# Performance work log

Hardware: AMD Instinct MI355X
Metric: run time of the kernel (lower is better)

Reference implementation:

```python
import jax, jax.numpy as jnp
import numpy as np

TOP_K = 2  # MoE top-k routing


def setup_inputs() -> dict:
    key = jax.random.key(0)
    ks = jax.random.split(key, 5)
    B, D, H, O, N = 8192, 3072, 128, 10, 8
    scale_g = 1.0 / np.sqrt(D)
    return {
        "x": jax.random.normal(ks[0], (B, D), dtype=jnp.float32),
        "Wg": jax.random.normal(ks[1], (D, N), dtype=jnp.float32) * scale_g,
        "bg": jnp.zeros((N,), dtype=jnp.float32),
        "W1": jax.random.normal(ks[2], (N, D, H), dtype=jnp.float32) * scale_g,
        "b1": jnp.zeros((N, H), dtype=jnp.float32),
        "W2": jax.random.normal(ks[3], (N, H, O), dtype=jnp.float32) * (1.0 / np.sqrt(H)),
        "b2": jnp.zeros((N, O), dtype=jnp.float32),
    }


def reference(x, Wg, bg, W1, b1, W2, b2):
    # Gating: logits -> top-k -> softmax over the k selected logits
    g = x @ Wg + bg                                  # [B, N]
    tv, ti = jax.lax.top_k(g, TOP_K)                 # [B, k]
    w = jax.nn.softmax(tv, axis=-1)                  # [B, k]
    # Expert MLPs, computed densely over all experts (vectorized dispatch)
    h = jax.nn.relu(jnp.einsum('bd,edh->beh', x, W1) + b1)   # [B, N, H]
    y = jnp.einsum('beh,eho->beo', h, W2) + b2               # [B, N, O]
    # Combine: gather each token's k selected expert outputs, weight, sum
    ysel = jnp.take_along_axis(y, ti[:, :, None], axis=1)    # [B, k, O]
    return jnp.sum(w[:, :, None] * ysel, axis=1)             # [B, O]
```

## Files before the change

### kernel.cpp

```cpp
#include <hip/hip_runtime.h>
#include <hip/hip_bf16.h>

#define B_TOK 8192
#define D_DIM 3072
#define H_DIM 128
#define O_DIM 10
#define N_EXP 8

#define BM 128
#define BK2 128
#define HLDS_STRIDE 136
#define ESTRIDE 4096

typedef __bf16 bf16x8 __attribute__((ext_vector_type(8)));
typedef float  f32x4  __attribute__((ext_vector_type(4)));
typedef unsigned short us8 __attribute__((ext_vector_type(8)));

__device__ __forceinline__ unsigned short f2bf(float f) {
  unsigned int u = __float_as_uint(f);
  unsigned int r = (u + 0x7FFFu + ((u >> 16) & 1u)) >> 16;
  return (unsigned short)r;
}

__device__ __forceinline__ void async16(const void* g, void* l) {
  __builtin_amdgcn_global_load_lds(
      (const __attribute__((address_space(1))) void*)g,
      (__attribute__((address_space(3))) void*)l,
      16, 0, 0);
}

__global__ __launch_bounds__(256) void k0_w1_transpose(const float* __restrict__ W1,
                                                       unsigned short* __restrict__ w1t) {
  __shared__ __align__(16) unsigned short lds[64 * 72];
  const int e  = blockIdx.z;
  const int d0 = blockIdx.x * 64;
  const int h0 = blockIdx.y * 64;
  const int tid = threadIdx.x;

  const float* src = W1 + ((size_t)e * D_DIM + d0) * H_DIM + h0;
  const int hl = tid & 63;
  const int dg = tid >> 6;
#pragma unroll
  for (int k = 0; k < 16; ++k) {
    const int d = dg + 4 * k;
    lds[hl * 72 + d] = f2bf(src[(size_t)d * H_DIM + hl]);
  }
  __syncthreads();

  unsigned short* dst = w1t + ((size_t)e * H_DIM + h0) * D_DIM + d0;
  const int q  = tid & 7;
  const int h1 = tid >> 3;
#pragma unroll
  for (int k = 0; k < 2; ++k) {
    const int h = h1 + 32 * k;
    const int d = q * 8;
    us8 v = *(const us8*)(lds + h * 72 + d);
    *(us8*)(dst + (size_t)h * D_DIM + d) = v;
  }
}

__global__ __launch_bounds__(256) void k1_gate(
    const float* __restrict__ x, const float* __restrict__ Wg,
    const float* __restrict__ bg,
    unsigned short* __restrict__ xb,
    int4* __restrict__ idx4, float2* __restrict__ wts,
    int* __restrict__ cnt, int* __restrict__ tlist) {
  __shared__ int lcnt[N_EXP], gbase[N_EXP];
  const int tid  = threadIdx.x;
  if (tid < N_EXP) lcnt[tid] = 0;
  __syncthreads();

  const int lane = tid & 63;
  const int wv   = tid >> 6;
  const int t0   = blockIdx.x * 16 + wv * 4;

  const float* xr0 = x + (size_t)(t0 + 0) * D_DIM;
  const float* xr1 = x + (size_t)(t0 + 1) * D_DIM;
  const float* xr2 = x + (size_t)(t0 + 2) * D_DIM;
  const float* xr3 = x + (size_t)(t0 + 3) * D_DIM;
  unsigned short* xw0 = xb + (size_t)(t0 + 0) * D_DIM;
  unsigned short* xw1 = xb + (size_t)(t0 + 1) * D_DIM;
  unsigned short* xw2 = xb + (size_t)(t0 + 2) * D_DIM;
  unsigned short* xw3 = xb + (size_t)(t0 + 3) * D_DIM;

  float acc[4][N_EXP];
#pragma unroll
  for (int t = 0; t < 4; ++t)
#pragma unroll
    for (int n = 0; n < N_EXP; ++n) acc[t][n] = 0.f;

  for (int grp = 0; grp < 3; ++grp) {
    float4 xv0[4], xv1[4], xv2[4], xv3[4];
#pragma unroll
    for (int s = 0; s < 4; ++s) {
      const int dl = (grp * 4 + s) * 256 + lane * 4;
      xv0[s] = *(const float4*)(xr0 + dl);
      xv1[s] = *(const float4*)(xr1 + dl);
      xv2[s] = *(const float4*)(xr2 + dl);
      xv3[s] = *(const float4*)(xr3 + dl);
    }
#pragma unroll
    for (int s = 0; s < 4; ++s) {
      const int dl = (grp * 4 + s) * 256 + lane * 4;
      const float4* wp = (const float4*)(Wg + (size_t)dl * N_EXP);
      float4 wa[4], wb[4];
#pragma unroll
      for (int j = 0; j < 4; ++j) { wa[j] = wp[2 * j]; wb[j] = wp[2 * j + 1]; }

      ushort4 p;
      p.x = f2bf(xv0[s].x); p.y = f2bf(xv0[s].y); p.z = f2bf(xv0[s].z); p.w = f2bf(xv0[s].w);
      *(ushort4*)(xw0 + dl) = p;
      p.x = f2bf(xv1[s].x); p.y = f2bf(xv1[s].y); p.z = f2bf(xv1[s].z); p.w = f2bf(xv1[s].w);
      *(ushort4*)(xw1 + dl) = p;
      p.x = f2bf(xv2[s].x); p.y = f2bf(xv2[s].y); p.z = f2bf(xv2[s].z); p.w = f2bf(xv2[s].w);
      *(ushort4*)(xw2 + dl) = p;
      p.x = f2bf(xv3[s].x); p.y = f2bf(xv3[s].y); p.z = f2bf(xv3[s].z); p.w = f2bf(xv3[s].w);
      *(ushort4*)(xw3 + dl) = p;

      float xe0[4] = {xv0[s].x, xv0[s].y, xv0[s].z, xv0[s].w};
      float xe1[4] = {xv1[s].x, xv1[s].y, xv1[s].z, xv1[s].w};
      float xe2[4] = {xv2[s].x, xv2[s].y, xv2[s].z, xv2[s].w};
      float xe3[4] = {xv3[s].x, xv3[s].y, xv3[s].z, xv3[s].w};
#pragma unroll
      for (int j = 0; j < 4; ++j) {
        acc[0][0] = fmaf(xe0[j], wa[j].x, acc[0][0]);
        acc[0][1] = fmaf(xe0[j], wa[j].y, acc[0][1]);
        acc[0][2] = fmaf(xe0[j], wa[j].z, acc[0][2]);
        acc[0][3] = fmaf(xe0[j], wa[j].w, acc[0][3]);
        acc[0][4] = fmaf(xe0[j], wb[j].x, acc[0][4]);
        acc[0][5] = fmaf(xe0[j], wb[j].y, acc[0][5]);
        acc[0][6] = fmaf(xe0[j], wb[j].z, acc[0][6]);
        acc[0][7] = fmaf(xe0[j], wb[j].w, acc[0][7]);
        acc[1][0] = fmaf(xe1[j], wa[j].x, acc[1][0]);
        acc[1][1] = fmaf(xe1[j], wa[j].y, acc[1][1]);
        acc[1][2] = fmaf(xe1[j], wa[j].z, acc[1][2]);
        acc[1][3] = fmaf(xe1[j], wa[j].w, acc[1][3]);
        acc[1][4] = fmaf(xe1[j], wb[j].x, acc[1][4]);
        acc[1][5] = fmaf(xe1[j], wb[j].y, acc[1][5]);
        acc[1][6] = fmaf(xe1[j], wb[j].z, acc[1][6]);
        acc[1][7] = fmaf(xe1[j], wb[j].w, acc[1][7]);
        acc[2][0] = fmaf(xe2[j], wa[j].x, acc[2][0]);
        acc[2][1] = fmaf(xe2[j], wa[j].y, acc[2][1]);
        acc[2][2] = fmaf(xe2[j], wa[j].z, acc[2][2]);
        acc[2][3] = fmaf(xe2[j], wa[j].w, acc[2][3]);
        acc[2][4] = fmaf(xe2[j], wb[j].x, acc[2][4]);
        acc[2][5] = fmaf(xe2[j], wb[j].y, acc[2][5]);
        acc[2][6] = fmaf(xe2[j], wb[j].z, acc[2][6]);
        acc[2][7] = fmaf(xe2[j], wb[j].w, acc[2][7]);
        acc[3][0] = fmaf(xe3[j], wa[j].x, acc[3][0]);
        acc[3][1] = fmaf(xe3[j], wa[j].y, acc[3][1]);
        acc[3][2] = fmaf(xe3[j], wa[j].z, acc[3][2]);
        acc[3][3] = fmaf(xe3[j], wa[j].w, acc[3][3]);
        acc[3][4] = fmaf(xe3[j], wb[j].x, acc[3][4]);
        acc[3][5] = fmaf(xe3[j], wb[j].y, acc[3][5]);
        acc[3][6] = fmaf(xe3[j], wb[j].z, acc[3][6]);
        acc[3][7] = fmaf(xe3[j], wb[j].w, acc[3][7]);
      }
    }
  }

#pragma unroll
  for (int t = 0; t < 4; ++t)
#pragma unroll
    for (int n = 0; n < N_EXP; ++n) {
#pragma unroll
      for (int off = 32; off > 0; off >>= 1)
        acc[t][n] += __shfl_xor(acc[t][n], off, 64);
    }

  int i0 = 0, i1 = 0, lp0 = 0, lp1 = 0;
  float w0 = 0.f, w1 = 0.f;
  if (lane < 4) {
    float g[N_EXP];
#pragma unroll
    for (int n = 0; n < N_EXP; ++n) {
      float v = acc[0][n];
      v = (lane == 1) ? acc[1][n] : v;
      v = (lane == 2) ? acc[2][n] : v;
      v = (lane == 3) ? acc[3][n] : v;
      g[n] = v + bg[n];
    }
    float m0 = g[0];
#pragma unroll
    for (int n = 1; n < N_EXP; ++n)
      if (g[n] > m0) { m0 = g[n]; i0 = n; }
    float m1 = -3.4e38f;
#pragma unroll
    for (int n = 0; n < N_EXP; ++n)
      if (n != i0 && g[n] > m1) { m1 = g[n]; i1 = n; }
    const float e1  = expf(m1 - m0);
    const float inv = 1.f / (1.f + e1);
    w0 = inv; w1 = e1 * inv;
    lp0 = atomicAdd(&lcnt[i0], 1);
    lp1 = atomicAdd(&lcnt[i1], 1);
  }
  __syncthreads();
  if (tid < N_EXP) gbase[tid] = atomicAdd(&cnt[tid], lcnt[tid]);
  __syncthreads();
  if (lane < 4) {
    const int t = t0 + lane;
    int p0 = gbase[i0] + lp0; p0 = p0 < ESTRIDE ? p0 : ESTRIDE - 1;
    int p1 = gbase[i1] + lp1; p1 = p1 < ESTRIDE ? p1 : ESTRIDE - 1;
    tlist[i0 * ESTRIDE + p0] = t;
    tlist[i1 * ESTRIDE + p1] = t;
    idx4[t] = make_int4(i0, p0, i1, p1);
    wts[t]  = make_float2(w0, w1);
  }
}

__global__ __launch_bounds__(256) void k2_experts(
    const unsigned short* __restrict__ xb,
    const unsigned short* __restrict__ w1t,
    const float* __restrict__ b1,
    const float* __restrict__ W2,
    const float* __restrict__ b2,
    const int* __restrict__ cnt, const int* __restrict__ tlist,
    float* __restrict__ ypair) {
  const int e    = blockIdx.y;
  int n_e        = cnt[e];
  n_e            = n_e < ESTRIDE ? n_e : ESTRIDE;
  const int row0 = blockIdx.x * BM;
  if (row0 >= n_e) return;

  __shared__ __align__(16) unsigned short sm[65536 + 2048];
  unsigned short* h_lds   = sm;
  unsigned short* w2t_lds = sm + 65536;

  const int tid  = threadIdx.x;
  const int lane = tid & 63;
  const int wv   = tid >> 6;
  const int quad = lane >> 4;
  const int cl   = lane & 15;

  const unsigned short* Abase[8];
  const unsigned short* Bbase[8];
#pragma unroll
  for (int j = 0; j < 8; ++j) {
    const int rloc = wv * 32 + j * 4 + quad;
    int gr = row0 + rloc;
    gr = gr < n_e ? gr : n_e - 1;
    const int koff = ((cl - (j * 4 + quad)) & 15) * 8;
    Abase[j] = xb + (size_t)tlist[e * ESTRIDE + gr] * D_DIM + koff;
    Bbase[j] = w1t + ((size_t)e * H_DIM + rloc) * D_DIM + koff;
  }

#define STAGE(it, pp)                                                     \
  {                                                                       \
    const int ko = (it) * BK2;                                            \
    unsigned short* abuf = sm + (pp) * 32768;                             \
    unsigned short* bbuf = sm + 16384 + (pp) * 32768;                     \
    _Pragma("unroll")                                                     \
    for (int j = 0; j < 8; ++j) {                                         \
      const int ldsrow = (wv * 32 + j * 4) * BK2;                         \
      async16(Abase[j] + ko, abuf + ldsrow);                              \
      async16(Bbase[j] + ko, bbuf + ldsrow);                              \
    }                                                                     \
  }

  STAGE(0, 0);

  const float* W2e = W2 + (size_t)e * H_DIM * O_DIM;
  for (int idx = tid; idx < 16 * 128; idx += 256) {
    const int o = idx >> 7, hh = idx & 127;
    const float v = (o < O_DIM) ? W2e[hh * O_DIM + o] : 0.f;
    w2t_lds[o * 128 + ((((hh >> 3) + o) & 15) * 8) + (hh & 7)] = f2bf(v);
  }

  const int mhalf = (wv >> 1) * 64;
  const int nhalf = (wv & 1) * 64;

  f32x4 acc[4][4];
#pragma unroll
  for (int i = 0; i < 4; ++i)
#pragma unroll
    for (int j = 0; j < 4; ++j)
      acc[i][j] = (f32x4){0.f, 0.f, 0.f, 0.f};

  const int NIT = D_DIM / BK2;
  for (int it = 0; it < NIT; ++it) {
    __syncthreads();
    if (it + 1 < NIT) STAGE(it + 1, (it + 1) & 1);
    const unsigned short* al = sm + (it & 1) * 32768;
    const unsigned short* bl = sm + 16384 + (it & 1) * 32768;
#pragma unroll
    for (int kk = 0; kk < 4; ++kk) {
      const int pos = ((kk * 4 + quad + cl) & 15) * 8;
      bf16x8 af[4], bfr[4];
#pragma unroll
      for (int mi = 0; mi < 4; ++mi)
        af[mi] = *(const bf16x8*)(al + (mhalf + mi * 16 + cl) * BK2 + pos);
#pragma unroll
      for (int ni = 0; ni < 4; ++ni)
        bfr[ni] = *(const bf16x8*)(bl + (nhalf + ni * 16 + cl) * BK2 + pos);
#pragma unroll
      for (int mi = 0; mi < 4; ++mi)
#pragma unroll
        for (int ni = 0; ni < 4; ++ni)
          acc[mi][ni] = __builtin_amdgcn_mfma_f32_16x16x32_bf16(af[mi], bfr[ni], acc[mi][ni], 0, 0, 0);
    }
  }
  __syncthreads();

  const float* b1e = b1 + e * H_DIM;
#pragma unroll
  for (int ni = 0; ni < 4; ++ni) {
    const int col  = nhalf + ni * 16 + cl;
    const float bias = b1e[col];
#pragma unroll
    for (int mi = 0; mi < 4; ++mi) {
      const int rbase = mhalf + mi * 16 + (quad << 2);
#pragma unroll
      for (int r = 0; r < 4; ++r) {
        float v = acc[mi][ni][r] + bias;
        v = v > 0.f ? v : 0.f;
        h_lds[(rbase + r) * HLDS_STRIDE + col] = f2bf(v);
      }
    }
  }
  __syncthreads();

  f32x4 acc2[2];
  acc2[0] = (f32x4){0.f, 0.f, 0.f, 0.f};
  acc2[1] = (f32x4){0.f, 0.f, 0.f, 0.f};
#pragma unroll
  for (int ks = 0; ks < 4; ++ks) {
    const int krd = ks * 32 + quad * 8;
    bf16x8 bfr = *(const bf16x8*)(w2t_lds + cl * 128 + ((ks * 4 + quad + cl) & 15) * 8);
#pragma unroll
    for (int mi = 0; mi < 2; ++mi) {
      bf16x8 afr = *(const bf16x8*)(h_lds + (wv * 32 + mi * 16 + cl) * HLDS_STRIDE + krd);
      acc2[mi] = __builtin_amdgcn_mfma_f32_16x16x32_bf16(afr, bfr, acc2[mi], 0, 0, 0);
    }
  }
  const int o = cl;
  if (o < O_DIM) {
    const float bias2 = b2[e * O_DIM + o];
#pragma unroll
    for (int mi = 0; mi < 2; ++mi) {
#pragma unroll
      for (int r = 0; r < 4; ++r) {
        const int rl = wv * 32 + mi * 16 + (quad << 2) + r;
        if (row0 + rl < n_e)
          ypair[(size_t)(e * ESTRIDE + row0 + rl) * 16 + o] = acc2[mi][r] + bias2;
      }
    }
  }
}

__global__ __launch_bounds__(256) void k3_combine(
    const float* __restrict__ ypair, const int4* __restrict__ idx4,
    const float2* __restrict__ wts, float* __restrict__ out) {
  const int g = blockIdx.x * 256 + threadIdx.x;
  if (g >= B_TOK * O_DIM) return;
  const int b = g / O_DIM, o = g - b * O_DIM;
  const int4 r = idx4[b];
  const float2 w = wts[b];
  out[g] = w.x * ypair[(size_t)(r.x * ESTRIDE + r.y) * 16 + o] +
           w.y * ypair[(size_t)(r.z * ESTRIDE + r.w) * 16 + o];
}

extern "C" void kernel_launch(void* const* d_in, const int* in_sizes, int n_in,
                              void* d_out, int out_size, void* d_ws, size_t ws_size,
                              hipStream_t stream) {
  const float* x  = (const float*)d_in[0];
  const float* Wg = (const float*)d_in[1];
  const float* bg = (const float*)d_in[2];
  const float* W1 = (const float*)d_in[3];
  const float* b1 = (const float*)d_in[4];
  const float* W2 = (const float*)d_in[5];
  const float* b2 = (const float*)d_in[6];
  float* out = (float*)d_out;

  char* ws = (char*)d_ws;
  unsigned short* xb  = (unsigned short*)ws;
  unsigned short* w1t = (unsigned short*)(ws + 50331648);
  int4*   idx4  = (int4*)  (ws + 56623104);
  float2* wts   = (float2*)(ws + 56754176);
  int*    cnt   = (int*)   (ws + 56819712);
  int*    tlist = (int*)   (ws + 56819840);
  float*  ypair = (float*) (ws + 56950912);

  k0_w1_transpose<<<dim3(48, 2, 8), dim3(256), 0, stream>>>(W1, w1t);
  (void)hipMemsetAsync(cnt, 0, N_EXP * sizeof(int), stream);
  k1_gate<<<dim3(B_TOK / 16), dim3(256), 0, stream>>>(
      x, Wg, bg, xb, idx4, wts, cnt, tlist);
  k2_experts<<<dim3(ESTRIDE / BM, N_EXP), dim3(256), 0, stream>>>(
      xb, w1t, b1, W2, b2, cnt, tlist, ypair);
  k3_combine<<<dim3((B_TOK * O_DIM + 255) / 256), dim3(256), 0, stream>>>(
      ypair, idx4, wts, out);
}
```

Measured before the change: 244.5 us.

## Merge W1 transpose into gate kernel and fuse combine via atomics

```diff
diff --git a/kernel.cpp b/kernel.cpp
--- a/kernel.cpp
+++ b/kernel.cpp
@@ -12,6 +12,9 @@
 #define HLDS_STRIDE 136
 #define ESTRIDE 4096
 
+#define K1_BLOCKS 512
+#define K0_BLOCKS 768
+
 typedef __bf16 bf16x8 __attribute__((ext_vector_type(8)));
 typedef float  f32x4  __attribute__((ext_vector_type(4)));
 typedef unsigned short us8 __attribute__((ext_vector_type(8)));
@@ -29,44 +32,48 @@
       16, 0, 0);
 }
 
-__global__ __launch_bounds__(256) void k0_w1_transpose(const float* __restrict__ W1,
-                                                       unsigned short* __restrict__ w1t) {
-  __shared__ __align__(16) unsigned short lds[64 * 72];
-  const int e  = blockIdx.z;
-  const int d0 = blockIdx.x * 64;
-  const int h0 = blockIdx.y * 64;
-  const int tid = threadIdx.x;
-
-  const float* src = W1 + ((size_t)e * D_DIM + d0) * H_DIM + h0;
-  const int hl = tid & 63;
-  const int dg = tid >> 6;
-#pragma unroll
-  for (int k = 0; k < 16; ++k) {
-    const int d = dg + 4 * k;
-    lds[hl * 72 + d] = f2bf(src[(size_t)d * H_DIM + hl]);
-  }
-  __syncthreads();
-
-  unsigned short* dst = w1t + ((size_t)e * H_DIM + h0) * D_DIM + d0;
-  const int q  = tid & 7;
-  const int h1 = tid >> 3;
-#pragma unroll
-  for (int k = 0; k < 2; ++k) {
-    const int h = h1 + 32 * k;
-    const int d = q * 8;
-    us8 v = *(const us8*)(lds + h * 72 + d);
-    *(us8*)(dst + (size_t)h * D_DIM + d) = v;
-  }
-}
-
-__global__ __launch_bounds__(256) void k1_gate(
+__global__ __launch_bounds__(256) void kA_gate_w1t(
     const float* __restrict__ x, const float* __restrict__ Wg,
     const float* __restrict__ bg,
+    const float* __restrict__ W1, unsigned short* __restrict__ w1t,
     unsigned short* __restrict__ xb,
-    int4* __restrict__ idx4, float2* __restrict__ wts,
-    int* __restrict__ cnt, int* __restrict__ tlist) {
-  __shared__ int lcnt[N_EXP], gbase[N_EXP];
-  const int tid  = threadIdx.x;
+    int* __restrict__ cnt, int* __restrict__ tlist, float* __restrict__ wslot) {
+  __shared__ __align__(16) char smem[64 * 72 * 2];
+  const int tid = threadIdx.x;
+
+  if (blockIdx.x >= K1_BLOCKS) {
+    unsigned short* lds = (unsigned short*)smem;
+    const int id = blockIdx.x - K1_BLOCKS;
+    const int e  = id / 96;
+    const int r  = id - e * 96;
+    const int h0 = (r / 48) * 64;
+    const int d0 = (r % 48) * 64;
+
+    const float* src = W1 + ((size_t)e * D_DIM + d0) * H_DIM + h0;
+    const int hl = tid & 63;
+    const int dg = tid >> 6;
+#pragma unroll
+    for (int k = 0; k < 16; ++k) {
+      const int d = dg + 4 * k;
+      lds[hl * 72 + d] = f2bf(src[(size_t)d * H_DIM + hl]);
+    }
+    __syncthreads();
+
+    unsigned short* dst = w1t + ((size_t)e * H_DIM + h0) * D_DIM + d0;
+    const int q  = tid & 7;
+    const int h1 = tid >> 3;
+#pragma unroll
+    for (int k = 0; k < 2; ++k) {
+      const int h = h1 + 32 * k;
+      const int d = q * 8;
+      us8 v = *(const us8*)(lds + h * 72 + d);
+      *(us8*)(dst + (size_t)h * D_DIM + d) = v;
+    }
+    return;
+  }
+
+  int* lcnt  = (int*)smem;
+  int* gbase = lcnt + N_EXP;
   if (tid < N_EXP) lcnt[tid] = 0;
   __syncthreads();
 
@@ -89,73 +96,65 @@
 #pragma unroll
     for (int n = 0; n < N_EXP; ++n) acc[t][n] = 0.f;
 
-  for (int grp = 0; grp < 3; ++grp) {
-    float4 xv0[4], xv1[4], xv2[4], xv3[4];
-#pragma unroll
-    for (int s = 0; s < 4; ++s) {
-      const int dl = (grp * 4 + s) * 256 + lane * 4;
-      xv0[s] = *(const float4*)(xr0 + dl);
-      xv1[s] = *(const float4*)(xr1 + dl);
-      xv2[s] = *(const float4*)(xr2 + dl);
-      xv3[s] = *(const float4*)(xr3 + dl);
-    }
-#pragma unroll
-    for (int s = 0; s < 4; ++s) {
-      const int dl = (grp * 4 + s) * 256 + lane * 4;
-      const float4* wp = (const float4*)(Wg + (size_t)dl * N_EXP);
-      float4 wa[4], wb[4];
-#pragma unroll
-      for (int j = 0; j < 4; ++j) { wa[j] = wp[2 * j]; wb[j] = wp[2 * j + 1]; }
-
-      ushort4 p;
-      p.x = f2bf(xv0[s].x); p.y = f2bf(xv0[s].y); p.z = f2bf(xv0[s].z); p.w = f2bf(xv0[s].w);
-      *(ushort4*)(xw0 + dl) = p;
-      p.x = f2bf(xv1[s].x); p.y = f2bf(xv1[s].y); p.z = f2bf(xv1[s].z); p.w = f2bf(xv1[s].w);
-      *(ushort4*)(xw1 + dl) = p;
-      p.x = f2bf(xv2[s].x); p.y = f2bf(xv2[s].y); p.z = f2bf(xv2[s].z); p.w = f2bf(xv2[s].w);
-      *(ushort4*)(xw2 + dl) = p;
-      p.x = f2bf(xv3[s].x); p.y = f2bf(xv3[s].y); p.z = f2bf(xv3[s].z); p.w = f2bf(xv3[s].w);
-      *(ushort4*)(xw3 + dl) = p;
-
-      float xe0[4] = {xv0[s].x, xv0[s].y, xv0[s].z, xv0[s].w};
-      float xe1[4] = {xv1[s].x, xv1[s].y, xv1[s].z, xv1[s].w};
-      float xe2[4] = {xv2[s].x, xv2[s].y, xv2[s].z, xv2[s].w};
-      float xe3[4] = {xv3[s].x, xv3[s].y, xv3[s].z, xv3[s].w};
-#pragma unroll
-      for (int j = 0; j < 4; ++j) {
-        acc[0][0] = fmaf(xe0[j], wa[j].x, acc[0][0]);
-        acc[0][1] = fmaf(xe0[j], wa[j].y, acc[0][1]);
-        acc[0][2] = fmaf(xe0[j], wa[j].z, acc[0][2]);
-        acc[0][3] = fmaf(xe0[j], wa[j].w, acc[0][3]);
-        acc[0][4] = fmaf(xe0[j], wb[j].x, acc[0][4]);
-        acc[0][5] = fmaf(xe0[j], wb[j].y, acc[0][5]);
-        acc[0][6] = fmaf(xe0[j], wb[j].z, acc[0][6]);
-        acc[0][7] = fmaf(xe0[j], wb[j].w, acc[0][7]);
-        acc[1][0] = fmaf(xe1[j], wa[j].x, acc[1][0]);
-        acc[1][1] = fmaf(xe1[j], wa[j].y, acc[1][1]);
-        acc[1][2] = fmaf(xe1[j], wa[j].z, acc[1][2]);
-        acc[1][3] = fmaf(xe1[j], wa[j].w, acc[1][3]);
-        acc[1][4] = fmaf(xe1[j], wb[j].x, acc[1][4]);
-        acc[1][5] = fmaf(xe1[j], wb[j].y, acc[1][5]);
-        acc[1][6] = fmaf(xe1[j], wb[j].z, acc[1][6]);
-        acc[1][7] = fmaf(xe1[j], wb[j].w, acc[1][7]);
-        acc[2][0] = fmaf(xe2[j], wa[j].x, acc[2][0]);
-        acc[2][1] = fmaf(xe2[j], wa[j].y, acc[2][1]);
-        acc[2][2] = fmaf(xe2[j], wa[j].z, acc[2][2]);
-        acc[2][3] = fmaf(xe2[j], wa[j].w, acc[2][3]);
-        acc[2][4] = fmaf(xe2[j], wb[j].x, acc[2][4]);
-        acc[2][5] = fmaf(xe2[j], wb[j].y, acc[2][5]);
-        acc[2][6] = fmaf(xe2[j], wb[j].z, acc[2][6]);
-        acc[2][7] = fmaf(xe2[j], wb[j].w, acc[2][7]);
-        acc[3][0] = fmaf(xe3[j], wa[j].x, acc[3][0]);
-        acc[3][1] = fmaf(xe3[j], wa[j].y, acc[3][1]);
-        acc[3][2] = fmaf(xe3[j], wa[j].z, acc[3][2]);
-        acc[3][3] = fmaf(xe3[j], wa[j].w, acc[3][3]);
-        acc[3][4] = fmaf(xe3[j], wb[j].x, acc[3][4]);
-        acc[3][5] = fmaf(xe3[j], wb[j].y, acc[3][5]);
-        acc[3][6] = fmaf(xe3[j], wb[j].z, acc[3][6]);
-        acc[3][7] = fmaf(xe3[j], wb[j].w, acc[3][7]);
-      }
+  for (int s = 0; s < 12; ++s) {
+    const int dl = s * 256 + lane * 4;
+    float4 xv0 = *(const float4*)(xr0 + dl);
+    float4 xv1 = *(const float4*)(xr1 + dl);
+    float4 xv2 = *(const float4*)(xr2 + dl);
+    float4 xv3 = *(const float4*)(xr3 + dl);
+    const float4* wp = (const float4*)(Wg + (size_t)dl * N_EXP);
+    float4 wa[4], wb[4];
+#pragma unroll
+    for (int j = 0; j < 4; ++j) { wa[j] = wp[2 * j]; wb[j] = wp[2 * j + 1]; }
+
+    ushort4 p;
+    p.x = f2bf(xv0.x); p.y = f2bf(xv0.y); p.z = f2bf(xv0.z); p.w = f2bf(xv0.w);
+    *(ushort4*)(xw0 + dl) = p;
+    p.x = f2bf(xv1.x); p.y = f2bf(xv1.y); p.z = f2bf(xv1.z); p.w = f2bf(xv1.w);
+    *(ushort4*)(xw1 + dl) = p;
+    p.x = f2bf(xv2.x); p.y = f2bf(xv2.y); p.z = f2bf(xv2.z); p.w = f2bf(xv2.w);
+    *(ushort4*)(xw2 + dl) = p;
+    p.x = f2bf(xv3.x); p.y = f2bf(xv3.y); p.z = f2bf(xv3.z); p.w = f2bf(xv3.w);
+    *(ushort4*)(xw3 + dl) = p;
+
+    float xe0[4] = {xv0.x, xv0.y, xv0.z, xv0.w};
+    float xe1[4] = {xv1.x, xv1.y, xv1.z, xv1.w};
+    float xe2[4] = {xv2.x, xv2.y, xv2.z, xv2.w};
+    float xe3[4] = {xv3.x, xv3.y, xv3.z, xv3.w};
+#pragma unroll
+    for (int j = 0; j < 4; ++j) {
+      acc[0][0] = fmaf(xe0[j], wa[j].x, acc[0][0]);
+      acc[0][1] = fmaf(xe0[j], wa[j].y, acc[0][1]);
+      acc[0][2] = fmaf(xe0[j], wa[j].z, acc[0][2]);
+      acc[0][3] = fmaf(xe0[j], wa[j].w, acc[0][3]);
+      acc[0][4] = fmaf(xe0[j], wb[j].x, acc[0][4]);
+      acc[0][5] = fmaf(xe0[j], wb[j].y, acc[0][5]);
+      acc[0][6] = fmaf(xe0[j], wb[j].z, acc[0][6]);
+      acc[0][7] = fmaf(xe0[j], wb[j].w, acc[0][7]);
+      acc[1][0] = fmaf(xe1[j], wa[j].x, acc[1][0]);
+      acc[1][1] = fmaf(xe1[j], wa[j].y, acc[1][1]);
+      acc[1][2] = fmaf(xe1[j], wa[j].z, acc[1][2]);
+      acc[1][3] = fmaf(xe1[j], wa[j].w, acc[1][3]);
+      acc[1][4] = fmaf(xe1[j], wb[j].x, acc[1][4]);
+      acc[1][5] = fmaf(xe1[j], wb[j].y, acc[1][5]);
+      acc[1][6] = fmaf(xe1[j], wb[j].z, acc[1][6]);
+      acc[1][7] = fmaf(xe1[j], wb[j].w, acc[1][7]);
+      acc[2][0] = fmaf(xe2[j], wa[j].x, acc[2][0]);
+      acc[2][1] = fmaf(xe2[j], wa[j].y, acc[2][1]);
+      acc[2][2] = fmaf(xe2[j], wa[j].z, acc[2][2]);
+      acc[2][3] = fmaf(xe2[j], wa[j].w, acc[2][3]);
+      acc[2][4] = fmaf(xe2[j], wb[j].x, acc[2][4]);
+      acc[2][5] = fmaf(xe2[j], wb[j].y, acc[2][5]);
+      acc[2][6] = fmaf(xe2[j], wb[j].z, acc[2][6]);
+      acc[2][7] = fmaf(xe2[j], wb[j].w, acc[2][7]);
+      acc[3][0] = fmaf(xe3[j], wa[j].x, acc[3][0]);
+      acc[3][1] = fmaf(xe3[j], wa[j].y, acc[3][1]);
+      acc[3][2] = fmaf(xe3[j], wa[j].z, acc[3][2]);
+      acc[3][3] = fmaf(xe3[j], wa[j].w, acc[3][3]);
+      acc[3][4] = fmaf(xe3[j], wb[j].x, acc[3][4]);
+      acc[3][5] = fmaf(xe3[j], wb[j].y, acc[3][5]);
+      acc[3][6] = fmaf(xe3[j], wb[j].z, acc[3][6]);
+      acc[3][7] = fmaf(xe3[j], wb[j].w, acc[3][7]);
     }
   }
 
@@ -203,8 +202,8 @@
     int p1 = gbase[i1] + lp1; p1 = p1 < ESTRIDE ? p1 : ESTRIDE - 1;
     tlist[i0 * ESTRIDE + p0] = t;
     tlist[i1 * ESTRIDE + p1] = t;
-    idx4[t] = make_int4(i0, p0, i1, p1);
-    wts[t]  = make_float2(w0, w1);
+    wslot[i0 * ESTRIDE + p0] = w0;
+    wslot[i1 * ESTRIDE + p1] = w1;
   }
 }
 
@@ -215,7 +214,8 @@
     const float* __restrict__ W2,
     const float* __restrict__ b2,
     const int* __restrict__ cnt, const int* __restrict__ tlist,
-    float* __restrict__ ypair) {
+    const float* __restrict__ wslot,
+    float* __restrict__ out) {
   const int e    = blockIdx.y;
   int n_e        = cnt[e];
   n_e            = n_e < ESTRIDE ? n_e : ESTRIDE;
@@ -340,23 +340,15 @@
 #pragma unroll
       for (int r = 0; r < 4; ++r) {
         const int rl = wv * 32 + mi * 16 + (quad << 2) + r;
-        if (row0 + rl < n_e)
-          ypair[(size_t)(e * ESTRIDE + row0 + rl) * 16 + o] = acc2[mi][r] + bias2;
+        const int slot = row0 + rl;
+        if (slot < n_e) {
+          const int t = tlist[e * ESTRIDE + slot];
+          const float w = wslot[e * ESTRIDE + slot];
+          atomicAdd(out + (size_t)t * O_DIM + o, w * (acc2[mi][r] + bias2));
+        }
       }
     }
   }
-}
-
-__global__ __launch_bounds__(256) void k3_combine(
-    const float* __restrict__ ypair, const int4* __restrict__ idx4,
-    const float2* __restrict__ wts, float* __restrict__ out) {
-  const int g = blockIdx.x * 256 + threadIdx.x;
-  if (g >= B_TOK * O_DIM) return;
-  const int b = g / O_DIM, o = g - b * O_DIM;
-  const int4 r = idx4[b];
-  const float2 w = wts[b];
-  out[g] = w.x * ypair[(size_t)(r.x * ESTRIDE + r.y) * 16 + o] +
-           w.y * ypair[(size_t)(r.z * ESTRIDE + r.w) * 16 + o];
 }
 
 extern "C" void kernel_launch(void* const* d_in, const int* in_sizes, int n_in,
@@ -374,18 +366,14 @@
   char* ws = (char*)d_ws;
   unsigned short* xb  = (unsigned short*)ws;
   unsigned short* w1t = (unsigned short*)(ws + 50331648);
-  int4*   idx4  = (int4*)  (ws + 56623104);
-  float2* wts   = (float2*)(ws + 56754176);
-  int*    cnt   = (int*)   (ws + 56819712);
-  int*    tlist = (int*)   (ws + 56819840);
-  float*  ypair = (float*) (ws + 56950912);
-
-  k0_w1_transpose<<<dim3(48, 2, 8), dim3(256), 0, stream>>>(W1, w1t);
+  int*    cnt   = (int*)   (ws + 56623104);
+  int*    tlist = (int*)   (ws + 56623232);
+  float*  wslot = (float*) (ws + 56754304);
+
   (void)hipMemsetAsync(cnt, 0, N_EXP * sizeof(int), stream);
-  k1_gate<<<dim3(B_TOK / 16), dim3(256), 0, stream>>>(
-      x, Wg, bg, xb, idx4, wts, cnt, tlist);
+  (void)hipMemsetAsync(out, 0, (size_t)B_TOK * O_DIM * sizeof(float), stream);
+  kA_gate_w1t<<<dim3(K1_BLOCKS + K0_BLOCKS), dim3(256), 0, stream>>>(
+      x, Wg, bg, W1, w1t, xb, cnt, tlist, wslot);
   k2_experts<<<dim3(ESTRIDE / BM, N_EXP), dim3(256), 0, stream>>>(
-      xb, w1t, b1, W2, b2, cnt, tlist, ypair);
-  k3_combine<<<dim3((B_TOK * O_DIM + 255) / 256), dim3(256), 0, stream>>>(
-      ypair, idx4, wts, out);
-}
+      xb, w1t, b1, W2, b2, cnt, tlist, wslot, out);
+}
```

Result: faster. 238.6 us (-2.4%).
